# Kernel tuning notes

Measured on AMD Instinct MI355X. Metric: run time of the kernel, lower is better.

The kernel has to match this reference:

```python
import jax, jax.numpy as jnp
import numpy as np

D_MODEL = 256
D_INNER = 512   # expand_factor * d_model
D_STATE = 64
DT_RANK = 4     # ceil(d_model / 64)
D_CONV = 4
B = 8
L = 144


def setup_inputs() -> dict:
    key = jax.random.key(0)
    ks = jax.random.split(key, 8)
    s = lambda k, shp, sc=0.02: jax.random.normal(k, shp, jnp.float32) * sc
    x = jax.random.normal(ks[0], (B, L, D_MODEL), jnp.float32)
    lastin = jnp.zeros((B, D_INNER, D_STATE), jnp.float32)  # accepted but unused by the scan
    W_in = s(ks[1], (2 * D_INNER, D_MODEL))              # in_proj (no bias)
    conv_w = s(ks[2], (D_INNER, 1, D_CONV), 0.1)          # depthwise conv kernel [O, I/groups, K]
    conv_b = jnp.zeros((D_INNER,), jnp.float32)
    W_x = s(ks[3], (DT_RANK + 2 * D_STATE, D_INNER))      # x_proj (no bias)
    W_dt = s(ks[4], (D_INNER, DT_RANK), 0.1)
    b_dt = jnp.full((D_INNER,), -4.0, jnp.float32)        # softplus -> small dt, like mamba init
    A_log = jnp.log(jnp.tile(jnp.arange(1, D_STATE + 1, dtype=jnp.float32), (D_INNER, 1)))
    Dp = jnp.ones((D_INNER,), jnp.float32)
    W_out = s(ks[5], (D_MODEL, D_INNER))                  # out_proj (no bias)
    return dict(x=x, lastin=lastin, W_in=W_in, conv_w=conv_w, conv_b=conv_b,
                W_x=W_x, W_dt=W_dt, b_dt=b_dt, A_log=A_log, Dp=Dp, W_out=W_out)


def _forward(x, lastin, W_in, conv_w, conv_b, W_x, W_dt, b_dt, A_log, Dp, W_out):
    # in_proj and split
    xz = jnp.einsum('bld,ed->ble', x, W_in)               # [B, L, 2*d_inner]
    ix, z = jnp.split(xz, 2, axis=-1)

    # depthwise causal-ish conv1d: torch padding=2 then slice [:L] == padding (2, 1)
    ix = jnp.swapaxes(ix, 1, 2)                            # [B, d_inner, L]
    ix = jax.lax.conv_general_dilated(
        ix, conv_w, window_strides=(1,), padding=[(2, 1)],
        feature_group_count=D_INNER, dimension_numbers=('NCH', 'OIH', 'NCH'))
    ix = ix + conv_b[None, :, None]
    ix = jnp.swapaxes(ix, 1, 2)                            # [B, L, d_inner]
    ix = jax.nn.silu(ix)

    # ssm parameterization
    A = -jnp.exp(A_log)                                    # [d_inner, d_state]
    dBC = jnp.einsum('bld,ed->ble', ix, W_x)               # [B, L, dt_rank + 2*d_state]
    dt_r = dBC[..., :DT_RANK]
    Bm = dBC[..., DT_RANK:DT_RANK + D_STATE]               # [B, L, d_state]
    Cm = dBC[..., DT_RANK + D_STATE:]                      # [B, L, d_state]
    delta = jax.nn.softplus(jnp.einsum('blr,dr->bld', dt_r, W_dt) + b_dt)  # [B, L, d_inner]

    # discretization
    deltaA = jnp.exp(delta[..., None] * A)                 # [B, L, d_inner, d_state]
    BX = (delta * ix)[..., None] * Bm[:, :, None, :]       # [B, L, d_inner, d_state]

    # sequential selective scan: h_t = deltaA_t * h_{t-1} + BX_t
    def step(h, inp):
        dA_t, bx_t = inp
        h = dA_t * h + bx_t
        return h, h

    h0 = jnp.zeros((x.shape[0], D_INNER, D_STATE), x.dtype)
    _, hs = jax.lax.scan(step, h0, (jnp.moveaxis(deltaA, 1, 0), jnp.moveaxis(BX, 1, 0)))
    # hs: [L, B, d_inner, d_state]

    y = jnp.einsum('lbdn,lbn->bld', hs, jnp.moveaxis(Cm, 1, 0))  # [B, L, d_inner]
    y = y + Dp * ix

    out = jnp.einsum('bld,ed->ble', y * jax.nn.silu(z), W_out)   # [B, L, d_model]
    return out


def reference(x, lastin, W_in, conv_w, conv_b, W_x, W_dt, b_dt, A_log, Dp, W_out):
    return _forward(x, lastin, W_in, conv_w, conv_b, W_x, W_dt, b_dt, A_log, Dp, W_out)
```

## Files before the change

kernel.cpp:

```cpp
#include <hip/hip_runtime.h>

#define B_SZ 8
#define L_SEQ 144
#define NTOK 1152
#define D_MODEL 256
#define D_INNER 512
#define D_STATE 64
#define DT_RANK 4
#define NDBC 132

#define BM 64
#define BN 64
#define BK 16

template<bool A_MK, bool GN, bool CONV>
__global__ __launch_bounds__(256) void gemm_k(const float* __restrict__ A,
                                              const float* __restrict__ Bm,
                                              float* __restrict__ C,
                                              const int N, const int lda, const int ldb,
                                              const int ldc,
                                              const float* __restrict__ cw,
                                              const float* __restrict__ cb,
                                              const int kslab, const size_t sstride) {
    __shared__ float As[BK][BM + 4];
    __shared__ float Bs[BK][BN + 4];
    const int tid = threadIdx.x;
    const int m0 = blockIdx.y * BM;
    const int n0 = blockIdx.x * BN;
    const int kbeg = blockIdx.z * kslab;
    const int kend = kbeg + kslab;
    const int ty = tid >> 4, tx = tid & 15;
    const int lrow = tid >> 2, kq = (tid & 3) * 4;
    const int kk = tid >> 4, cc = (tid & 15) * 4;
    float acc[4][4] = {};
    float4 av, bv, cw4;
    float xm2 = 0.f, xm1 = 0.f, xp4 = 0.f, cbv = 0.f;

    auto loadA = [&](const int k0) {
        if (A_MK) {
            av = *(const float4*)(A + (size_t)(m0 + lrow) * lda + k0 + kq);
        } else {
            const float* row = A + (size_t)(k0 + kk) * lda + m0 + cc;
            av = *(const float4*)row;
            if (CONV) {
                const int t = (m0 + cc) % L_SEQ;
                xm2 = (t > 0) ? row[-2] : 0.f;
                xm1 = (t > 0) ? row[-1] : 0.f;
                xp4 = (t < L_SEQ - 4) ? row[4] : 0.f;
                cw4 = *(const float4*)(cw + (k0 + kk) * 4);
                cbv = cb[k0 + kk];
            }
        }
        if (!GN || (n0 + lrow) < N)
            bv = *(const float4*)(Bm + (size_t)(n0 + lrow) * ldb + k0 + kq);
    };

    auto storeLDS = [&]() {
        if (A_MK) {
            As[kq + 0][lrow] = av.x; As[kq + 1][lrow] = av.y;
            As[kq + 2][lrow] = av.z; As[kq + 3][lrow] = av.w;
        } else if (CONV) {
            const float in7[7] = {xm2, xm1, av.x, av.y, av.z, av.w, xp4};
            float4 o;
            float* op = &o.x;
#pragma unroll
            for (int j = 0; j < 4; ++j) {
                float s = cbv;
                s = fmaf(cw4.x, in7[j + 0], s);
                s = fmaf(cw4.y, in7[j + 1], s);
                s = fmaf(cw4.z, in7[j + 2], s);
                s = fmaf(cw4.w, in7[j + 3], s);
                op[j] = s * __builtin_amdgcn_rcpf(1.f + __expf(-s));
            }
            *(float4*)&As[kk][cc] = o;
        } else {
            *(float4*)&As[kk][cc] = av;
        }
        Bs[kq + 0][lrow] = bv.x; Bs[kq + 1][lrow] = bv.y;
        Bs[kq + 2][lrow] = bv.z; Bs[kq + 3][lrow] = bv.w;
    };

    bv = make_float4(0.f, 0.f, 0.f, 0.f);
    loadA(kbeg);
    for (int k0 = kbeg; k0 < kend; k0 += BK) {
        __syncthreads();
        storeLDS();
        __syncthreads();
        if (k0 + BK < kend) loadA(k0 + BK);
#pragma unroll
        for (int k = 0; k < BK; ++k) {
            const float4 a4 = *(const float4*)&As[k][ty * 4];
            const float4 b4 = *(const float4*)&Bs[k][tx * 4];
            const float a_[4] = {a4.x, a4.y, a4.z, a4.w};
            const float b_[4] = {b4.x, b4.y, b4.z, b4.w};
#pragma unroll
            for (int i = 0; i < 4; ++i)
#pragma unroll
                for (int j = 0; j < 4; ++j)
                    acc[i][j] = fmaf(a_[i], b_[j], acc[i][j]);
        }
    }
    C += (size_t)blockIdx.z * sstride;
#pragma unroll
    for (int i = 0; i < 4; ++i) {
        const int gm = m0 + ty * 4 + i;
        const int gn = n0 + tx * 4;
        if (!GN || gn < N)
            *(float4*)(C + (size_t)gm * ldc + gn) =
                make_float4(acc[i][0], acc[i][1], acc[i][2], acc[i][3]);
    }
}

__global__ __launch_bounds__(256) void reduce4_k(const float4* __restrict__ in,
                                                 float4* __restrict__ out,
                                                 const int n4, const int s4) {
    const int i = blockIdx.x * 256 + threadIdx.x;
    if (i >= n4) return;
    const float4 a = in[i], b = in[i + s4], c = in[i + 2 * s4], d = in[i + 3 * s4];
    out[i] = make_float4(a.x + b.x + c.x + d.x, a.y + b.y + c.y + d.y,
                         a.z + b.z + c.z + d.z, a.w + b.w + c.w + d.w);
}

template<int CNT>
__device__ __forceinline__ void scan_chunk(const float* __restrict__ dBC,
                                           const float* __restrict__ xzT,
                                           float* __restrict__ gT,
                                           float4* __restrict__ aux_w,
                                           float (*__restrict__ Pw)[65],
                                           const int d, const int base, const int t0,
                                           const float An2, const float4 wdt,
                                           const float bdt, const float dpv,
                                           const float4 cw4, const float cbv,
                                           const int lane, float& h) {
    if (lane < CNT) {
        const int t = t0 + lane;
        const int tok = base + t;
        const float* row = xzT + (size_t)d * NTOK + tok;
        float s0 = cbv;
        if (t >= 2) s0 = fmaf(cw4.x, row[-2], s0);
        if (t >= 1) s0 = fmaf(cw4.y, row[-1], s0);
        s0 = fmaf(cw4.z, row[0], s0);
        if (t < L_SEQ - 1) s0 = fmaf(cw4.w, row[1], s0);
        const float ixv = s0 * __builtin_amdgcn_rcpf(1.f + __expf(-s0));

        const float4 dt4 = *(const float4*)(dBC + (size_t)tok * NDBC);
        float s = fmaf(dt4.x, wdt.x, bdt);
        s = fmaf(dt4.y, wdt.y, s);
        s = fmaf(dt4.z, wdt.z, s);
        s = fmaf(dt4.w, wdt.w, s);
        const float delta = fmaxf(s, 0.f) + __logf(1.f + __expf(-fabsf(s)));
        const float zv = xzT[(size_t)(D_INNER + d) * NTOK + tok];
        const float sz = zv * __builtin_amdgcn_rcpf(1.f + __expf(-zv));
        aux_w[lane] = make_float4(delta, delta * ixv, dpv * ixv, sz);
    }
#pragma unroll 8
    for (int i = 0; i < CNT; ++i) {
        const size_t rb = (size_t)(base + t0 + i) * NDBC;
        const float Bv = dBC[rb + DT_RANK + lane];
        const float Cv = dBC[rb + DT_RANK + D_STATE + lane];
        const float4 a4 = aux_w[i];
        const float dA = __builtin_amdgcn_exp2f(a4.x * An2);
        h = fmaf(dA, h, a4.y * Bv);
        Pw[i][lane] = h * Cv;
    }
    const int tl = lane & 31, hf = lane >> 5;
    float s2 = 0.f;
    if (tl < CNT) {
#pragma unroll
        for (int j = 0; j < 32; ++j) s2 += Pw[tl][hf * 32 + j];
    }
    s2 += __shfl_xor(s2, 32, 64);
    if (hf == 0 && tl < CNT) {
        const float4 a4 = aux_w[tl];
        gT[(size_t)d * NTOK + base + t0 + tl] = (s2 + a4.z) * a4.w;
    }
}

__global__ __launch_bounds__(256) void scan_k(const float* __restrict__ dBC,
                                              const float* __restrict__ xzT,
                                              const float* __restrict__ W_dt,
                                              const float* __restrict__ b_dt,
                                              const float* __restrict__ A_log,
                                              const float* __restrict__ Dp,
                                              const float* __restrict__ conv_w,
                                              const float* __restrict__ conv_b,
                                              float* __restrict__ gT) {
    __shared__ float4 aux_s[4][32];
    __shared__ float P[4][32][65];
    const int w = threadIdx.x >> 6, lane = threadIdx.x & 63;
    const int b = blockIdx.x >> 7, dg = blockIdx.x & 127;
    const int d = (dg << 2) | w;
    const int base = b * L_SEQ;
    const float An2 = -__expf(A_log[(d << 6) + lane]) * 1.44269504088896f;
    const float4 wdt = *(const float4*)(W_dt + (d << 2));
    const float bdt = b_dt[d], dpv = Dp[d];
    const float4 cw4 = *(const float4*)(conv_w + (d << 2));
    const float cbv = conv_b[d];
    float h = 0.f;
    scan_chunk<32>(dBC, xzT, gT, aux_s[w], P[w], d, base, 0,   An2, wdt, bdt, dpv, cw4, cbv, lane, h);
    scan_chunk<32>(dBC, xzT, gT, aux_s[w], P[w], d, base, 32,  An2, wdt, bdt, dpv, cw4, cbv, lane, h);
    scan_chunk<32>(dBC, xzT, gT, aux_s[w], P[w], d, base, 64,  An2, wdt, bdt, dpv, cw4, cbv, lane, h);
    scan_chunk<32>(dBC, xzT, gT, aux_s[w], P[w], d, base, 96,  An2, wdt, bdt, dpv, cw4, cbv, lane, h);
    scan_chunk<16>(dBC, xzT, gT, aux_s[w], P[w], d, base, 128, An2, wdt, bdt, dpv, cw4, cbv, lane, h);
}

extern "C" void kernel_launch(void* const* d_in, const int* in_sizes, int n_in,
                              void* d_out, int out_size, void* d_ws, size_t ws_size,
                              hipStream_t stream) {
    const float* x      = (const float*)d_in[0];
    const float* W_in   = (const float*)d_in[2];
    const float* conv_w = (const float*)d_in[3];
    const float* conv_b = (const float*)d_in[4];
    const float* W_x    = (const float*)d_in[5];
    const float* W_dt   = (const float*)d_in[6];
    const float* b_dt   = (const float*)d_in[7];
    const float* A_log  = (const float*)d_in[8];
    const float* Dp     = (const float*)d_in[9];
    const float* W_out  = (const float*)d_in[10];
    float* out = (float*)d_out;

    float* ws  = (float*)d_ws;
    float* xzT = ws;
    float* dBC = xzT + 1179648;
    float* gT  = dBC + 152064;
    float* sl3 = gT + 589824;
    float* sl6 = xzT;

    gemm_k<true, false, false><<<dim3(18, 16, 1), 256, 0, stream>>>(
        W_in, x, xzT, NTOK, D_MODEL, D_MODEL, NTOK, nullptr, nullptr, D_MODEL, 0);
    gemm_k<false, true, true><<<dim3(3, 18, 4), 256, 0, stream>>>(
        xzT, W_x, sl3, NDBC, NTOK, D_INNER, NDBC, conv_w, conv_b, 128,
        (size_t)NTOK * NDBC);
    reduce4_k<<<dim3(149), 256, 0, stream>>>((const float4*)sl3, (float4*)dBC,
                                             NTOK * NDBC / 4, NTOK * NDBC / 4);
    scan_k<<<dim3(B_SZ * 128), 256, 0, stream>>>(dBC, xzT, W_dt, b_dt, A_log, Dp,
                                                 conv_w, conv_b, gT);
    gemm_k<false, false, false><<<dim3(4, 18, 4), 256, 0, stream>>>(
        gT, W_out, sl6, D_MODEL, NTOK, D_INNER, D_MODEL, nullptr, nullptr, 128,
        (size_t)NTOK * D_MODEL);
    reduce4_k<<<dim3(288), 256, 0, stream>>>((const float4*)sl6, (float4*)out,
                                             NTOK * D_MODEL / 4, NTOK * D_MODEL / 4);
}
```

Baseline: 138.7 us.

## Drop split-K reduce kernels: fold x_proj reduction into scan, new out_proj GEMM

Removes both reduce4 launches. The scan now sums the four split-K partial slabs of the x_proj output inline when it reads dt, B and C. The out_proj split-K GEMM plus its reduction is replaced by a single non-split GEMM with narrow 16-column tiles over the full K, 288 blocks writing the output directly. This saves two launches and the intermediate round trips through memory. In exchange the scan's inner loop does four times as many global loads for B and C, and the new GEMM does more serial K work per block.

```diff
diff --git a/kernel.cpp b/kernel.cpp
--- a/kernel.cpp
+++ b/kernel.cpp
@@ -8,10 +8,12 @@
 #define D_STATE 64
 #define DT_RANK 4
 #define NDBC 132
+#define SLAB 152064
 
 #define BM 64
 #define BN 64
 #define BK 16
+#define BN3 16
 
 template<bool A_MK, bool GN, bool CONV>
 __global__ __launch_bounds__(256) void gemm_k(const float* __restrict__ A,
@@ -111,18 +113,52 @@
     }
 }
 
-__global__ __launch_bounds__(256) void reduce4_k(const float4* __restrict__ in,
-                                                 float4* __restrict__ out,
-                                                 const int n4, const int s4) {
-    const int i = blockIdx.x * 256 + threadIdx.x;
-    if (i >= n4) return;
-    const float4 a = in[i], b = in[i + s4], c = in[i + 2 * s4], d = in[i + 3 * s4];
-    out[i] = make_float4(a.x + b.x + c.x + d.x, a.y + b.y + c.y + d.y,
-                         a.z + b.z + c.z + d.z, a.w + b.w + c.w + d.w);
+__global__ __launch_bounds__(256) void gemm3_k(const float* __restrict__ A,
+                                               const float* __restrict__ Bw,
+                                               float* __restrict__ C) {
+    __shared__ float As[64][BM + 4];
+    __shared__ float Bs[64][BN3 + 4];
+    const int tid = threadIdx.x;
+    const int m0 = blockIdx.y * BM;
+    const int n0 = blockIdx.x * BN3;
+    const int kk = tid >> 4, cc = (tid & 15) * 4;
+    const int bn = tid >> 4, bk = (tid & 15) * 4;
+    const int r = tid >> 2, c4 = (tid & 3) * 4;
+    float4 acc = make_float4(0.f, 0.f, 0.f, 0.f);
+    float4 av[4], bv;
+
+    auto load = [&](const int k0) {
+#pragma unroll
+        for (int j = 0; j < 4; ++j)
+            av[j] = *(const float4*)(A + (size_t)(k0 + kk + 16 * j) * NTOK + m0 + cc);
+        bv = *(const float4*)(Bw + (size_t)(n0 + bn) * D_INNER + k0 + bk);
+    };
+
+    load(0);
+    for (int k0 = 0; k0 < D_INNER; k0 += 64) {
+        __syncthreads();
+#pragma unroll
+        for (int j = 0; j < 4; ++j)
+            *(float4*)&As[kk + 16 * j][cc] = av[j];
+        Bs[bk + 0][bn] = bv.x; Bs[bk + 1][bn] = bv.y;
+        Bs[bk + 2][bn] = bv.z; Bs[bk + 3][bn] = bv.w;
+        __syncthreads();
+        if (k0 + 64 < D_INNER) load(k0 + 64);
+#pragma unroll
+        for (int k = 0; k < 64; ++k) {
+            const float a = As[k][r];
+            const float4 b4 = *(const float4*)&Bs[k][c4];
+            acc.x = fmaf(a, b4.x, acc.x);
+            acc.y = fmaf(a, b4.y, acc.y);
+            acc.z = fmaf(a, b4.z, acc.z);
+            acc.w = fmaf(a, b4.w, acc.w);
+        }
+    }
+    *(float4*)(C + (size_t)(m0 + r) * D_MODEL + n0 + c4) = acc;
 }
 
 template<int CNT>
-__device__ __forceinline__ void scan_chunk(const float* __restrict__ dBC,
+__device__ __forceinline__ void scan_chunk(const float* __restrict__ sl3,
                                            const float* __restrict__ xzT,
                                            float* __restrict__ gT,
                                            float4* __restrict__ aux_w,
@@ -143,11 +179,19 @@
         if (t < L_SEQ - 1) s0 = fmaf(cw4.w, row[1], s0);
         const float ixv = s0 * __builtin_amdgcn_rcpf(1.f + __expf(-s0));
 
-        const float4 dt4 = *(const float4*)(dBC + (size_t)tok * NDBC);
-        float s = fmaf(dt4.x, wdt.x, bdt);
-        s = fmaf(dt4.y, wdt.y, s);
-        s = fmaf(dt4.z, wdt.z, s);
-        s = fmaf(dt4.w, wdt.w, s);
+        const float* q = sl3 + (size_t)tok * NDBC;
+        const float4 q0 = *(const float4*)(q);
+        const float4 q1 = *(const float4*)(q + SLAB);
+        const float4 q2 = *(const float4*)(q + 2 * SLAB);
+        const float4 q3 = *(const float4*)(q + 3 * SLAB);
+        const float dtx = q0.x + q1.x + q2.x + q3.x;
+        const float dty = q0.y + q1.y + q2.y + q3.y;
+        const float dtz = q0.z + q1.z + q2.z + q3.z;
+        const float dtw = q0.w + q1.w + q2.w + q3.w;
+        float s = fmaf(dtx, wdt.x, bdt);
+        s = fmaf(dty, wdt.y, s);
+        s = fmaf(dtz, wdt.z, s);
+        s = fmaf(dtw, wdt.w, s);
         const float delta = fmaxf(s, 0.f) + __logf(1.f + __expf(-fabsf(s)));
         const float zv = xzT[(size_t)(D_INNER + d) * NTOK + tok];
         const float sz = zv * __builtin_amdgcn_rcpf(1.f + __expf(-zv));
@@ -155,9 +199,10 @@
     }
 #pragma unroll 8
     for (int i = 0; i < CNT; ++i) {
-        const size_t rb = (size_t)(base + t0 + i) * NDBC;
-        const float Bv = dBC[rb + DT_RANK + lane];
-        const float Cv = dBC[rb + DT_RANK + D_STATE + lane];
+        const float* p = sl3 + (size_t)(base + t0 + i) * NDBC + DT_RANK + lane;
+        const float Bv = p[0] + p[SLAB] + p[2 * SLAB] + p[3 * SLAB];
+        const float Cv = p[D_STATE] + p[SLAB + D_STATE] + p[2 * SLAB + D_STATE]
+                       + p[3 * SLAB + D_STATE];
         const float4 a4 = aux_w[i];
         const float dA = __builtin_amdgcn_exp2f(a4.x * An2);
         h = fmaf(dA, h, a4.y * Bv);
@@ -176,7 +221,7 @@
     }
 }
 
-__global__ __launch_bounds__(256) void scan_k(const float* __restrict__ dBC,
+__global__ __launch_bounds__(256) void scan_k(const float* __restrict__ sl3,
                                               const float* __restrict__ xzT,
                                               const float* __restrict__ W_dt,
                                               const float* __restrict__ b_dt,
@@ -197,11 +242,11 @@
     const float4 cw4 = *(const float4*)(conv_w + (d << 2));
     const float cbv = conv_b[d];
     float h = 0.f;
-    scan_chunk<32>(dBC, xzT, gT, aux_s[w], P[w], d, base, 0,   An2, wdt, bdt, dpv, cw4, cbv, lane, h);
-    scan_chunk<32>(dBC, xzT, gT, aux_s[w], P[w], d, base, 32,  An2, wdt, bdt, dpv, cw4, cbv, lane, h);
-    scan_chunk<32>(dBC, xzT, gT, aux_s[w], P[w], d, base, 64,  An2, wdt, bdt, dpv, cw4, cbv, lane, h);
-    scan_chunk<32>(dBC, xzT, gT, aux_s[w], P[w], d, base, 96,  An2, wdt, bdt, dpv, cw4, cbv, lane, h);
-    scan_chunk<16>(dBC, xzT, gT, aux_s[w], P[w], d, base, 128, An2, wdt, bdt, dpv, cw4, cbv, lane, h);
+    scan_chunk<32>(sl3, xzT, gT, aux_s[w], P[w], d, base, 0,   An2, wdt, bdt, dpv, cw4, cbv, lane, h);
+    scan_chunk<32>(sl3, xzT, gT, aux_s[w], P[w], d, base, 32,  An2, wdt, bdt, dpv, cw4, cbv, lane, h);
+    scan_chunk<32>(sl3, xzT, gT, aux_s[w], P[w], d, base, 64,  An2, wdt, bdt, dpv, cw4, cbv, lane, h);
+    scan_chunk<32>(sl3, xzT, gT, aux_s[w], P[w], d, base, 96,  An2, wdt, bdt, dpv, cw4, cbv, lane, h);
+    scan_chunk<16>(sl3, xzT, gT, aux_s[w], P[w], d, base, 128, An2, wdt, bdt, dpv, cw4, cbv, lane, h);
 }
 
 extern "C" void kernel_launch(void* const* d_in, const int* in_sizes, int n_in,
@@ -221,23 +266,15 @@
 
     float* ws  = (float*)d_ws;
     float* xzT = ws;
-    float* dBC = xzT + 1179648;
-    float* gT  = dBC + 152064;
-    float* sl3 = gT + 589824;
-    float* sl6 = xzT;
+    float* sl3 = xzT + 1179648;
+    float* gT  = sl3 + 4 * SLAB;
 
     gemm_k<true, false, false><<<dim3(18, 16, 1), 256, 0, stream>>>(
         W_in, x, xzT, NTOK, D_MODEL, D_MODEL, NTOK, nullptr, nullptr, D_MODEL, 0);
     gemm_k<false, true, true><<<dim3(3, 18, 4), 256, 0, stream>>>(
         xzT, W_x, sl3, NDBC, NTOK, D_INNER, NDBC, conv_w, conv_b, 128,
-        (size_t)NTOK * NDBC);
-    reduce4_k<<<dim3(149), 256, 0, stream>>>((const float4*)sl3, (float4*)dBC,
-                                             NTOK * NDBC / 4, NTOK * NDBC / 4);
-    scan_k<<<dim3(B_SZ * 128), 256, 0, stream>>>(dBC, xzT, W_dt, b_dt, A_log, Dp,
+        (size_t)SLAB);
+    scan_k<<<dim3(B_SZ * 128), 256, 0, stream>>>(sl3, xzT, W_dt, b_dt, A_log, Dp,
                                                  conv_w, conv_b, gT);
-    gemm_k<false, false, false><<<dim3(4, 18, 4), 256, 0, stream>>>(
-        gT, W_out, sl6, D_MODEL, NTOK, D_INNER, D_MODEL, nullptr, nullptr, 128,
-        (size_t)NTOK * D_MODEL);
-    reduce4_k<<<dim3(288), 256, 0, stream>>>((const float4*)sl6, (float4*)out,
-                                             NTOK * D_MODEL / 4, NTOK * D_MODEL / 4);
-}
+    gemm3_k<<<dim3(16, 18), 256, 0, stream>>>(gT, W_out, out);
+}
```

Measured after the change: 175.9 us. +26.9%, slower.

## Interleave B/C columns in dBC and broadcast scan aux values via readlane

Applied to the files above, without the earlier changes.

The x_proj GEMM now reads W_x rows in a permuted order, so its output stores B and C interleaved per state index. The scan can then fetch both with one float2 load per lane per step instead of two scalar loads. The per-timestep delta and delta*x values stay in registers and are broadcast with readlane, which removes the LDS aux buffer and its loads. The scan loop is now fully unrolled, which may raise register pressure.

```diff
diff --git a/kernel.cpp b/kernel.cpp
--- a/kernel.cpp
+++ b/kernel.cpp
@@ -8,12 +8,19 @@
 #define D_STATE 64
 #define DT_RANK 4
 #define NDBC 132
+#define SLAB 152064
 
 #define BM 64
 #define BN 64
 #define BK 16
 
-template<bool A_MK, bool GN, bool CONV>
+__device__ __forceinline__ int bc_perm(const int p) {
+    return (p < DT_RANK) ? p
+         : (((p - DT_RANK) & 1) ? (DT_RANK + D_STATE + ((p - DT_RANK) >> 1))
+                                : (DT_RANK + ((p - DT_RANK) >> 1)));
+}
+
+template<bool A_MK, bool GN, bool CONV, bool PERM>
 __global__ __launch_bounds__(256) void gemm_k(const float* __restrict__ A,
                                               const float* __restrict__ Bm,
                                               float* __restrict__ C,
@@ -32,6 +39,7 @@
     const int ty = tid >> 4, tx = tid & 15;
     const int lrow = tid >> 2, kq = (tid & 3) * 4;
     const int kk = tid >> 4, cc = (tid & 15) * 4;
+    const int brow = PERM ? bc_perm(n0 + lrow) : (n0 + lrow);
     float acc[4][4] = {};
     float4 av, bv, cw4;
     float xm2 = 0.f, xm1 = 0.f, xp4 = 0.f, cbv = 0.f;
@@ -52,7 +60,7 @@
             }
         }
         if (!GN || (n0 + lrow) < N)
-            bv = *(const float4*)(Bm + (size_t)(n0 + lrow) * ldb + k0 + kq);
+            bv = *(const float4*)(Bm + (size_t)brow * ldb + k0 + kq);
     };
 
     auto storeLDS = [&]() {
@@ -121,17 +129,21 @@
                          a.z + b.z + c.z + d.z, a.w + b.w + c.w + d.w);
 }
 
+__device__ __forceinline__ float bcast(const float v, const int i) {
+    return __int_as_float(__builtin_amdgcn_readlane(__float_as_int(v), i));
+}
+
 template<int CNT>
 __device__ __forceinline__ void scan_chunk(const float* __restrict__ dBC,
                                            const float* __restrict__ xzT,
                                            float* __restrict__ gT,
-                                           float4* __restrict__ aux_w,
                                            float (*__restrict__ Pw)[65],
                                            const int d, const int base, const int t0,
                                            const float An2, const float4 wdt,
                                            const float bdt, const float dpv,
                                            const float4 cw4, const float cbv,
                                            const int lane, float& h) {
+    float delta_r = 0.f, dix_r = 0.f, dpix_r = 0.f, sz_r = 0.f;
     if (lane < CNT) {
         const int t = t0 + lane;
         const int tok = base + t;
@@ -150,18 +162,20 @@
         s = fmaf(dt4.w, wdt.w, s);
         const float delta = fmaxf(s, 0.f) + __logf(1.f + __expf(-fabsf(s)));
         const float zv = xzT[(size_t)(D_INNER + d) * NTOK + tok];
-        const float sz = zv * __builtin_amdgcn_rcpf(1.f + __expf(-zv));
-        aux_w[lane] = make_float4(delta, delta * ixv, dpv * ixv, sz);
-    }
-#pragma unroll 8
+        delta_r = delta;
+        dix_r   = delta * ixv;
+        dpix_r  = dpv * ixv;
+        sz_r    = zv * __builtin_amdgcn_rcpf(1.f + __expf(-zv));
+    }
+#pragma unroll
     for (int i = 0; i < CNT; ++i) {
-        const size_t rb = (size_t)(base + t0 + i) * NDBC;
-        const float Bv = dBC[rb + DT_RANK + lane];
-        const float Cv = dBC[rb + DT_RANK + D_STATE + lane];
-        const float4 a4 = aux_w[i];
-        const float dA = __builtin_amdgcn_exp2f(a4.x * An2);
-        h = fmaf(dA, h, a4.y * Bv);
-        Pw[i][lane] = h * Cv;
+        const float2 bc = *(const float2*)(dBC + (size_t)(base + t0 + i) * NDBC
+                                           + DT_RANK + 2 * lane);
+        const float dlt = bcast(delta_r, i);
+        const float dxv = bcast(dix_r, i);
+        const float dA = __builtin_amdgcn_exp2f(dlt * An2);
+        h = fmaf(dA, h, dxv * bc.x);
+        Pw[i][lane] = h * bc.y;
     }
     const int tl = lane & 31, hf = lane >> 5;
     float s2 = 0.f;
@@ -171,8 +185,7 @@
     }
     s2 += __shfl_xor(s2, 32, 64);
     if (hf == 0 && tl < CNT) {
-        const float4 a4 = aux_w[tl];
-        gT[(size_t)d * NTOK + base + t0 + tl] = (s2 + a4.z) * a4.w;
+        gT[(size_t)d * NTOK + base + t0 + tl] = (s2 + dpix_r) * sz_r;
     }
 }
 
@@ -185,7 +198,6 @@
                                               const float* __restrict__ conv_w,
                                               const float* __restrict__ conv_b,
                                               float* __restrict__ gT) {
-    __shared__ float4 aux_s[4][32];
     __shared__ float P[4][32][65];
     const int w = threadIdx.x >> 6, lane = threadIdx.x & 63;
     const int b = blockIdx.x >> 7, dg = blockIdx.x & 127;
@@ -197,11 +209,11 @@
     const float4 cw4 = *(const float4*)(conv_w + (d << 2));
     const float cbv = conv_b[d];
     float h = 0.f;
-    scan_chunk<32>(dBC, xzT, gT, aux_s[w], P[w], d, base, 0,   An2, wdt, bdt, dpv, cw4, cbv, lane, h);
-    scan_chunk<32>(dBC, xzT, gT, aux_s[w], P[w], d, base, 32,  An2, wdt, bdt, dpv, cw4, cbv, lane, h);
-    scan_chunk<32>(dBC, xzT, gT, aux_s[w], P[w], d, base, 64,  An2, wdt, bdt, dpv, cw4, cbv, lane, h);
-    scan_chunk<32>(dBC, xzT, gT, aux_s[w], P[w], d, base, 96,  An2, wdt, bdt, dpv, cw4, cbv, lane, h);
-    scan_chunk<16>(dBC, xzT, gT, aux_s[w], P[w], d, base, 128, An2, wdt, bdt, dpv, cw4, cbv, lane, h);
+    scan_chunk<32>(dBC, xzT, gT, P[w], d, base, 0,   An2, wdt, bdt, dpv, cw4, cbv, lane, h);
+    scan_chunk<32>(dBC, xzT, gT, P[w], d, base, 32,  An2, wdt, bdt, dpv, cw4, cbv, lane, h);
+    scan_chunk<32>(dBC, xzT, gT, P[w], d, base, 64,  An2, wdt, bdt, dpv, cw4, cbv, lane, h);
+    scan_chunk<32>(dBC, xzT, gT, P[w], d, base, 96,  An2, wdt, bdt, dpv, cw4, cbv, lane, h);
+    scan_chunk<16>(dBC, xzT, gT, P[w], d, base, 128, An2, wdt, bdt, dpv, cw4, cbv, lane, h);
 }
 
 extern "C" void kernel_launch(void* const* d_in, const int* in_sizes, int n_in,
@@ -226,16 +238,15 @@
     float* sl3 = gT + 589824;
     float* sl6 = xzT;
 
-    gemm_k<true, false, false><<<dim3(18, 16, 1), 256, 0, stream>>>(
+    gemm_k<true, false, false, false><<<dim3(18, 16, 1), 256, 0, stream>>>(
         W_in, x, xzT, NTOK, D_MODEL, D_MODEL, NTOK, nullptr, nullptr, D_MODEL, 0);
-    gemm_k<false, true, true><<<dim3(3, 18, 4), 256, 0, stream>>>(
-        xzT, W_x, sl3, NDBC, NTOK, D_INNER, NDBC, conv_w, conv_b, 128,
-        (size_t)NTOK * NDBC);
+    gemm_k<false, true, true, true><<<dim3(3, 18, 4), 256, 0, stream>>>(
+        xzT, W_x, sl3, NDBC, NTOK, D_INNER, NDBC, conv_w, conv_b, 128, (size_t)SLAB);
     reduce4_k<<<dim3(149), 256, 0, stream>>>((const float4*)sl3, (float4*)dBC,
                                              NTOK * NDBC / 4, NTOK * NDBC / 4);
     scan_k<<<dim3(B_SZ * 128), 256, 0, stream>>>(dBC, xzT, W_dt, b_dt, A_log, Dp,
                                                  conv_w, conv_b, gT);
-    gemm_k<false, false, false><<<dim3(4, 18, 4), 256, 0, stream>>>(
+    gemm_k<false, false, false, false><<<dim3(4, 18, 4), 256, 0, stream>>>(
         gT, W_out, sl6, D_MODEL, NTOK, D_INNER, D_MODEL, nullptr, nullptr, 128,
         (size_t)NTOK * D_MODEL);
     reduce4_k<<<dim3(288), 256, 0, stream>>>((const float4*)sl6, (float4*)out,
```

Measured after the change: 141.6 us. 1.02x slower.
